# Optimization experiments

Measured on AMD Instinct MI355X. Metric: run time of the kernel, lower is better.

Reference implementation:

```python
import jax, jax.numpy as jnp
import numpy as np

B, NF, V, D, NI = 16384, 26, 100000, 16, 13
HID = [512, 256, 128, 64, 1]

def setup_inputs() -> dict:
    key = jax.random.key(0)
    ks = jax.random.split(key, 24)
    x_int = jax.random.normal(ks[0], (B, NI), dtype=jnp.float32)
    x_cat = jax.random.randint(ks[1], (B, NF), 0, V, dtype=jnp.int64)
    emb_tables = jax.random.normal(ks[2], (NF, V, D), dtype=jnp.float32) * 0.01
    lin_tables = jax.random.normal(ks[3], (NF, V, 1), dtype=jnp.float32) * 0.01
    W_num = jax.random.normal(ks[4], (NI, 1), dtype=jnp.float32) * 0.1
    b_num = jnp.zeros((1,), dtype=jnp.float32)
    bias = jnp.zeros((1,), dtype=jnp.float32)
    dims = [NF * D + NI] + HID  # 429 -> 512 -> 256 -> 128 -> 64 -> 1
    mlp = {}
    for li in range(5):
        fan_in = dims[li]
        mlp[f'W{li+1}'] = jax.random.normal(ks[5 + 2*li], (dims[li], dims[li+1]), dtype=jnp.float32) / np.sqrt(fan_in)
        mlp[f'b{li+1}'] = jnp.zeros((dims[li+1],), dtype=jnp.float32)
    return dict(x_int=x_int, x_cat=x_cat, emb_tables=emb_tables, lin_tables=lin_tables,
                W_num=W_num, b_num=b_num, bias=bias, **mlp)

def reference(x_int, x_cat, emb_tables, lin_tables, W_num, b_num, bias,
              W1, b1, W2, b2, W3, b3, W4, b4, W5, b5):
    feat_idx = jnp.arange(NF)[None, :]                 # [1, NF]
    emb = emb_tables[feat_idx, x_cat]                  # [B, NF, D] fused gather
    # FM second-order interaction
    sum_emb = jnp.sum(emb, axis=1)                     # [B, D]
    square_of_sum = sum_emb ** 2
    sum_of_square = jnp.sum(emb ** 2, axis=1)
    fm_score = 0.5 * jnp.sum(square_of_sum - sum_of_square, axis=1, keepdims=True)  # [B,1]
    # linear terms
    lin_cat_score = jnp.sum(lin_tables[feat_idx, x_cat], axis=1)  # [B,1]
    lin_num_score = x_int @ W_num + b_num                          # [B,1]
    # deep MLP (dropout is identity at inference)
    deep_in = jnp.concatenate([emb.reshape(emb.shape[0], -1), x_int], axis=1)  # [B, NF*D+NI]
    h = jax.nn.relu(deep_in @ W1 + b1)
    h = jax.nn.relu(h @ W2 + b2)
    h = jax.nn.relu(h @ W3 + b3)
    h = jax.nn.relu(h @ W4 + b4)
    deep_score = h @ W5 + b5                                       # [B,1]
    return bias + lin_cat_score + lin_num_score + fm_score + deep_score
```

## Files before the change

### kernel.cpp

```cpp
#include <hip/hip_runtime.h>
#include <hip/hip_bf16.h>
#include <stdint.h>

typedef __bf16 bf16x8 __attribute__((ext_vector_type(8)));
typedef float  f32x4  __attribute__((ext_vector_type(4)));

#define NROWS 16384
#define NFEAT 26
#define VOCAB 100000

__device__ __forceinline__ void convW(const float* __restrict__ W, __bf16* __restrict__ Wt,
                                      int K, int N, int Kpad, int i) {
  int n = i / Kpad, k = i - n * Kpad;
  float v = (k < K) ? W[(size_t)k * N + n] : 0.f;
  Wt[i] = (__bf16)v;
}

__global__ __launch_bounds__(256) void k_convAll(
    const float* __restrict__ W1, const float* __restrict__ W2,
    const float* __restrict__ W3, const float* __restrict__ W4,
    __bf16* __restrict__ Wt1, __bf16* __restrict__ Wt2,
    __bf16* __restrict__ Wt3, __bf16* __restrict__ Wt4) {
  int i = blockIdx.x * 256 + threadIdx.x;
  if (i < 229376)          convW(W1, Wt1, 429, 512, 448, i);
  else if (i < 360448)     convW(W2, Wt2, 512, 256, 512, i - 229376);
  else if (i < 393216)     convW(W3, Wt3, 256, 128, 256, i - 360448);
  else if (i < 401408)     convW(W4, Wt4, 128, 64, 128, i - 393216);
}

template<int K, int N, int NCT>
__device__ __forceinline__ void mlp_layer(const __bf16* __restrict__ Wt,
                                          const float* __restrict__ bias,
                                          const __bf16* Ain, __bf16* Aout,
                                          int w, int lane) {
  constexpr int LDA = K + 8, LDO = N + 8;
  const int lrow = lane & 15;
  const int kg = (lane >> 4) * 8;

  f32x4 acc[NCT][4];
  #pragma unroll
  for (int j = 0; j < NCT; ++j)
    #pragma unroll
    for (int m = 0; m < 4; ++m)
      #pragma unroll
      for (int i = 0; i < 4; ++i) acc[j][m][i] = 0.f;

  const __bf16* wp[NCT];
  #pragma unroll
  for (int j = 0; j < NCT; ++j)
    wp[j] = Wt + (size_t)((w + j * 8) * 16 + lrow) * K + kg;

  for (int k0 = 0; k0 < K; k0 += 32) {
    bf16x8 af[4];
    #pragma unroll
    for (int m = 0; m < 4; ++m)
      af[m] = *(const bf16x8*)(Ain + (m * 16 + lrow) * LDA + k0 + kg);
    bf16x8 bf[NCT];
    #pragma unroll
    for (int j = 0; j < NCT; ++j)
      bf[j] = *(const bf16x8*)(wp[j] + k0);
    #pragma unroll
    for (int j = 0; j < NCT; ++j)
      #pragma unroll
      for (int m = 0; m < 4; ++m)
        acc[j][m] = __builtin_amdgcn_mfma_f32_16x16x32_bf16(af[m], bf[j], acc[j][m], 0, 0, 0);
  }

  const int rbase = (lane >> 4) * 4;
  #pragma unroll
  for (int j = 0; j < NCT; ++j) {
    int col = (w + j * 8) * 16 + lrow;
    float bv = bias[col];
    #pragma unroll
    for (int m = 0; m < 4; ++m)
      #pragma unroll
      for (int i = 0; i < 4; ++i) {
        float v = acc[j][m][i] + bv;
        v = fmaxf(v, 0.f);
        Aout[(m * 16 + rbase + i) * LDO + col] = (__bf16)v;
      }
  }
}

__global__ __launch_bounds__(512) void k_fused(
    const float* __restrict__ x_int,
    const int*   __restrict__ x_cat,
    const float* __restrict__ emb,
    const float* __restrict__ lin,
    const float* __restrict__ W_num,
    const float* __restrict__ b_num,
    const float* __restrict__ bias0,
    const __bf16* __restrict__ Wt1, const float* __restrict__ b1,
    const __bf16* __restrict__ Wt2, const float* __restrict__ b2,
    const __bf16* __restrict__ Wt3, const float* __restrict__ b3,
    const __bf16* __restrict__ Wt4, const float* __restrict__ b4,
    const float* __restrict__ W5, const float* __restrict__ b5,
    float* __restrict__ out) {
  __shared__ __align__(16) char smem[125184];
  __bf16* A0 = (__bf16*)smem;
  __bf16* A1 = (__bf16*)(smem + 58368);
  int* s_idx = (int*)(smem + 58368);
  float* s_part = (float*)(smem + 124928);

  const int t = threadIdx.x;
  const int row0 = blockIdx.x * 64;
  const int w = t >> 6, lane = t & 63;

  for (int i = t; i < 64 * NFEAT; i += 512) {
    int r = i / NFEAT, f = i - r * NFEAT;
    s_idx[i] = x_cat[(size_t)(row0 + r) * NFEAT + f];
  }
  __syncthreads();

  const float pbias = bias0[0] + b_num[0];
  #pragma unroll
  for (int pp = 0; pp < 2; ++pp) {
    const int p = t + pp * 512;
    const int r = p >> 4, d = p & 15;
    float sum = 0.f, sumsq = 0.f;
    #pragma unroll
    for (int f = 0; f < NFEAT; ++f) {
      int idx = s_idx[r * NFEAT + f];
      float e = emb[((size_t)f * VOCAB + idx) * 16 + d];
      sum += e; sumsq += e * e;
      A0[r * 456 + f * 16 + d] = (__bf16)e;
    }
    float xv = (d < 13) ? x_int[(size_t)(row0 + r) * 13 + d] : 0.f;
    A0[r * 456 + 416 + d] = (__bf16)xv;
    A0[r * 456 + 432 + d] = (__bf16)0.f;

    float lin_s = lin[(size_t)d * VOCAB + s_idx[r * NFEAT + d]];
    if (d < NFEAT - 16)
      lin_s += lin[(size_t)(d + 16) * VOCAB + s_idx[r * NFEAT + d + 16]];
    float lin_num = (d < 13) ? xv * W_num[d] : 0.f;

    float red = 0.5f * (sum * sum - sumsq) + lin_s + lin_num;
    #pragma unroll
    for (int off = 1; off < 16; off <<= 1) red += __shfl_xor(red, off, 16);
    if (d == 0) s_part[r] = red + pbias;
  }
  __syncthreads();

  mlp_layer<448, 512, 4>(Wt1, b1, A0, A1, w, lane);
  __syncthreads();
  mlp_layer<512, 256, 2>(Wt2, b2, A1, A0, w, lane);
  __syncthreads();
  mlp_layer<256, 128, 1>(Wt3, b3, A0, A1, w, lane);
  __syncthreads();
  if (w < 4) mlp_layer<128, 64, 1>(Wt4, b4, A1, A0, w, lane);
  __syncthreads();

  {
    const int r = t >> 3, g = t & 7;
    bf16x8 hv = *(const bf16x8*)(A0 + r * 72 + g * 8);
    float s = 0.f;
    #pragma unroll
    for (int i = 0; i < 8; ++i) s += (float)hv[i] * W5[g * 8 + i];
    #pragma unroll
    for (int off = 1; off < 8; off <<= 1) s += __shfl_xor(s, off, 8);
    if (g == 0) out[row0 + r] = s + b5[0] + s_part[r];
  }
}

extern "C" void kernel_launch(void* const* d_in, const int* in_sizes, int n_in,
                              void* d_out, int out_size, void* d_ws, size_t ws_size,
                              hipStream_t stream) {
  const float* x_int = (const float*)d_in[0];
  const int*   x_cat = (const int*)d_in[1];
  const float* emb   = (const float*)d_in[2];
  const float* lin   = (const float*)d_in[3];
  const float* W_num = (const float*)d_in[4];
  const float* b_num = (const float*)d_in[5];
  const float* bias  = (const float*)d_in[6];
  const float* W1 = (const float*)d_in[7];  const float* b1 = (const float*)d_in[8];
  const float* W2 = (const float*)d_in[9];  const float* b2 = (const float*)d_in[10];
  const float* W3 = (const float*)d_in[11]; const float* b3 = (const float*)d_in[12];
  const float* W4 = (const float*)d_in[13]; const float* b4 = (const float*)d_in[14];
  const float* W5 = (const float*)d_in[15]; const float* b5 = (const float*)d_in[16];
  float* out = (float*)d_out;

  char* ws = (char*)d_ws;
  __bf16* Wt1 = (__bf16*)(ws);
  __bf16* Wt2 = (__bf16*)(ws + 458752);
  __bf16* Wt3 = (__bf16*)(ws + 720896);
  __bf16* Wt4 = (__bf16*)(ws + 786432);

  k_convAll<<<1568, 256, 0, stream>>>(W1, W2, W3, W4, Wt1, Wt2, Wt3, Wt4);

  k_fused<<<NROWS / 64, 512, 0, stream>>>(x_int, x_cat, emb, lin, W_num, b_num, bias,
                                          Wt1, b1, Wt2, b2, Wt3, b3, Wt4, b4, W5, b5,
                                          out);
}
```

Before: 52.97 us.

## Double fused-kernel block to 1024 threads and tile weight transpose via shared memory

```diff
diff --git a/kernel.cpp b/kernel.cpp
--- a/kernel.cpp
+++ b/kernel.cpp
@@ -9,11 +9,24 @@
 #define NFEAT 26
 #define VOCAB 100000
 
-__device__ __forceinline__ void convW(const float* __restrict__ W, __bf16* __restrict__ Wt,
-                                      int K, int N, int Kpad, int i) {
-  int n = i / Kpad, k = i - n * Kpad;
-  float v = (k < K) ? W[(size_t)k * N + n] : 0.f;
-  Wt[i] = (__bf16)v;
+__device__ __forceinline__ void transpose_tile(const float* __restrict__ W,
+                                               __bf16* __restrict__ Wt,
+                                               int K, int N, int Kpad,
+                                               int kt, int nt, int t) {
+  __shared__ float tile[32][33];
+  const int tx = t & 31, ty = t >> 5;
+  const int k0 = kt * 32, n0 = nt * 32;
+  #pragma unroll
+  for (int j = 0; j < 4; ++j) {
+    int k = k0 + ty + j * 8;
+    tile[ty + j * 8][tx] = (k < K) ? W[(size_t)k * N + n0 + tx] : 0.f;
+  }
+  __syncthreads();
+  #pragma unroll
+  for (int j = 0; j < 4; ++j) {
+    int n = n0 + ty + j * 8;
+    Wt[(size_t)n * Kpad + k0 + tx] = (__bf16)tile[tx][ty + j * 8];
+  }
 }
 
 __global__ __launch_bounds__(256) void k_convAll(
@@ -21,14 +34,14 @@
     const float* __restrict__ W3, const float* __restrict__ W4,
     __bf16* __restrict__ Wt1, __bf16* __restrict__ Wt2,
     __bf16* __restrict__ Wt3, __bf16* __restrict__ Wt4) {
-  int i = blockIdx.x * 256 + threadIdx.x;
-  if (i < 229376)          convW(W1, Wt1, 429, 512, 448, i);
-  else if (i < 360448)     convW(W2, Wt2, 512, 256, 512, i - 229376);
-  else if (i < 393216)     convW(W3, Wt3, 256, 128, 256, i - 360448);
-  else if (i < 401408)     convW(W4, Wt4, 128, 64, 128, i - 393216);
-}
-
-template<int K, int N, int NCT>
+  const int b = blockIdx.x, t = threadIdx.x;
+  if (b < 224)       { int i = b;        transpose_tile(W1, Wt1, 429, 512, 448, i % 14, i / 14, t); }
+  else if (b < 352)  { int i = b - 224;  transpose_tile(W2, Wt2, 512, 256, 512, i % 16, i / 16, t); }
+  else if (b < 384)  { int i = b - 352;  transpose_tile(W3, Wt3, 256, 128, 256, i % 8,  i / 8,  t); }
+  else               { int i = b - 384;  transpose_tile(W4, Wt4, 128,  64, 128, i % 4,  i / 4,  t); }
+}
+
+template<int K, int N, int NCT, int WS>
 __device__ __forceinline__ void mlp_layer(const __bf16* __restrict__ Wt,
                                           const float* __restrict__ bias,
                                           const __bf16* Ain, __bf16* Aout,
@@ -48,7 +61,7 @@
   const __bf16* wp[NCT];
   #pragma unroll
   for (int j = 0; j < NCT; ++j)
-    wp[j] = Wt + (size_t)((w + j * 8) * 16 + lrow) * K + kg;
+    wp[j] = Wt + (size_t)((w + j * WS) * 16 + lrow) * K + kg;
 
   for (int k0 = 0; k0 < K; k0 += 32) {
     bf16x8 af[4];
@@ -69,7 +82,7 @@
   const int rbase = (lane >> 4) * 4;
   #pragma unroll
   for (int j = 0; j < NCT; ++j) {
-    int col = (w + j * 8) * 16 + lrow;
+    int col = (w + j * WS) * 16 + lrow;
     float bv = bias[col];
     #pragma unroll
     for (int m = 0; m < 4; ++m)
@@ -82,7 +95,7 @@
   }
 }
 
-__global__ __launch_bounds__(512) void k_fused(
+__global__ __launch_bounds__(1024) void k_fused(
     const float* __restrict__ x_int,
     const int*   __restrict__ x_cat,
     const float* __restrict__ emb,
@@ -106,17 +119,15 @@
   const int row0 = blockIdx.x * 64;
   const int w = t >> 6, lane = t & 63;
 
-  for (int i = t; i < 64 * NFEAT; i += 512) {
+  for (int i = t; i < 64 * NFEAT; i += 1024) {
     int r = i / NFEAT, f = i - r * NFEAT;
     s_idx[i] = x_cat[(size_t)(row0 + r) * NFEAT + f];
   }
   __syncthreads();
 
-  const float pbias = bias0[0] + b_num[0];
-  #pragma unroll
-  for (int pp = 0; pp < 2; ++pp) {
-    const int p = t + pp * 512;
-    const int r = p >> 4, d = p & 15;
+  {
+    const float pbias = bias0[0] + b_num[0];
+    const int r = t >> 4, d = t & 15;
     float sum = 0.f, sumsq = 0.f;
     #pragma unroll
     for (int f = 0; f < NFEAT; ++f) {
@@ -141,23 +152,23 @@
   }
   __syncthreads();
 
-  mlp_layer<448, 512, 4>(Wt1, b1, A0, A1, w, lane);
-  __syncthreads();
-  mlp_layer<512, 256, 2>(Wt2, b2, A1, A0, w, lane);
-  __syncthreads();
-  mlp_layer<256, 128, 1>(Wt3, b3, A0, A1, w, lane);
-  __syncthreads();
-  if (w < 4) mlp_layer<128, 64, 1>(Wt4, b4, A1, A0, w, lane);
+  mlp_layer<448, 512, 2, 16>(Wt1, b1, A0, A1, w, lane);
+  __syncthreads();
+  mlp_layer<512, 256, 1, 16>(Wt2, b2, A1, A0, w, lane);
+  __syncthreads();
+  if (w < 8) mlp_layer<256, 128, 1, 8>(Wt3, b3, A0, A1, w, lane);
+  __syncthreads();
+  if (w < 4) mlp_layer<128, 64, 1, 4>(Wt4, b4, A1, A0, w, lane);
   __syncthreads();
 
   {
-    const int r = t >> 3, g = t & 7;
-    bf16x8 hv = *(const bf16x8*)(A0 + r * 72 + g * 8);
+    const int r = t >> 4, g = t & 15;
     float s = 0.f;
     #pragma unroll
-    for (int i = 0; i < 8; ++i) s += (float)hv[i] * W5[g * 8 + i];
-    #pragma unroll
-    for (int off = 1; off < 8; off <<= 1) s += __shfl_xor(s, off, 8);
+    for (int i = 0; i < 4; ++i)
+      s += (float)A0[r * 72 + g * 4 + i] * W5[g * 4 + i];
+    #pragma unroll
+    for (int off = 1; off < 16; off <<= 1) s += __shfl_xor(s, off, 16);
     if (g == 0) out[row0 + r] = s + b5[0] + s_part[r];
   }
 }
@@ -185,9 +196,9 @@
   __bf16* Wt3 = (__bf16*)(ws + 720896);
   __bf16* Wt4 = (__bf16*)(ws + 786432);
 
-  k_convAll<<<1568, 256, 0, stream>>>(W1, W2, W3, W4, Wt1, Wt2, Wt3, Wt4);
-
-  k_fused<<<NROWS / 64, 512, 0, stream>>>(x_int, x_cat, emb, lin, W_num, b_num, bias,
-                                          Wt1, b1, Wt2, b2, Wt3, b3, Wt4, b4, W5, b5,
-                                          out);
-}
+  k_convAll<<<392, 256, 0, stream>>>(W1, W2, W3, W4, Wt1, Wt2, Wt3, Wt4);
+
+  k_fused<<<NROWS / 64, 1024, 0, stream>>>(x_int, x_cat, emb, lin, W_num, b_num, bias,
+                                           Wt1, b1, Wt2, b2, Wt3, b3, Wt4, b4, W5, b5,
+                                           out);
+}
```

Result: faster. 51.18 us (-3.4%).
